# Kernel tuning notes

Measured on AMD Instinct MI355X. Metric: run time of the kernel, lower is better.

The kernel has to match this reference:

```python
import jax, jax.numpy as jnp
import numpy as np

N_NODES = 50000
N_EDGES = 1600000
F_IN, F_HID, F_MID = 264, 48, 64


def setup_inputs() -> dict:
    key = jax.random.key(0)
    ks = jax.random.split(key, 12)
    def lin(kw, fan_in, fan_out):
        s = 1.0 / np.sqrt(fan_in)
        return jax.random.uniform(kw, (fan_in, fan_out), jnp.float32, -s, s)
    return {
        "x": jax.random.normal(ks[0], (N_NODES, F_IN), jnp.float32),
        "edge_index": jax.random.randint(ks[1], (2, N_EDGES), 0, N_NODES, jnp.int64),
        "edge_weight": jax.random.uniform(ks[2], (N_EDGES,), jnp.float32, 0.01, 1.0),
        "WM": lin(ks[3], F_IN, F_HID), "bM": jnp.zeros((F_HID,), jnp.float32),
        "WA": lin(ks[4], F_IN, F_HID), "bA": jnp.zeros((F_HID,), jnp.float32),
        "WS": lin(ks[5], F_IN, F_HID), "bS": jnp.zeros((F_HID,), jnp.float32),
        "W1": lin(ks[6], 3 * F_HID, F_MID), "b1": jnp.zeros((F_MID,), jnp.float32),
        "W2": lin(ks[7], F_MID, 1), "b2": jnp.zeros((1,), jnp.float32),
    }


def _gcn_norm(edge_index, edge_weight, n):
    # add self-loops with weight 1 (PyG gcn_norm default)
    loop = jnp.arange(n, dtype=edge_index.dtype)
    row = jnp.concatenate([edge_index[0], loop])
    col = jnp.concatenate([edge_index[1], loop])
    w = jnp.concatenate([edge_weight, jnp.ones((n,), edge_weight.dtype)])
    deg = jax.ops.segment_sum(w, col, num_segments=n)
    dis = jnp.where(deg > 0, jax.lax.rsqrt(jnp.where(deg > 0, deg, 1.0)), 0.0)
    norm = dis[row] * w * dis[col]
    return row, col, norm


def reference(x, edge_index, edge_weight, WM, bM, WA, bA, WS, bS, W1, b1, W2, b2):
    n = x.shape[0]
    row, col, norm = _gcn_norm(edge_index, edge_weight, n)

    # GCNConv aggr='max': linear (no bias) -> gather -> weighted scatter-max -> +bias
    hM = x @ WM                              # [N, 48]
    msgM = norm[:, None] * hM[row]           # [E+N, 48]
    outM = jax.ops.segment_max(msgM, col, num_segments=n) + bM
    xConvM = jax.nn.relu(outM)

    # GCNConv aggr='add'
    hA = x @ WA
    msgA = norm[:, None] * hA[row]
    outA = jax.ops.segment_sum(msgA, col, num_segments=n) + bA
    xConvA = jax.nn.relu(outA)

    # plain linear branch
    xLin = jax.nn.relu(x @ WS + bS)

    h = jnp.concatenate([xConvM, xConvA, xLin], axis=1)  # [N, 144]
    h = jax.nn.relu(h @ W1 + b1)
    out = h @ W2 + b2                         # [N, 1]
    return out.squeeze(-1)
```

## Files before the change

kernel.cpp:

```cpp
#include <hip/hip_runtime.h>
#include <stdint.h>

#define N_NODES 50000
#define N_EDGES 1600000
#define F_IN    264
#define F_HID   48
#define F_CAT   144
#define F_MID   64
#define K_PAD   288
#define K_MLP   160

#define BSH     6
#define NB      782
#define CHUNK   4096
#define NCHUNK  ((N_EDGES + CHUNK - 1) / CHUNK)

typedef unsigned short u16;
typedef unsigned int   u32;

using short8  = __attribute__((ext_vector_type(8))) short;
using floatx4 = __attribute__((ext_vector_type(4))) float;
using floatx2 = __attribute__((ext_vector_type(2))) float;
using uintx4  = __attribute__((ext_vector_type(4))) u32;

__device__ __forceinline__ float bf2f(u16 u) {
    return __uint_as_float(((u32)u) << 16);
}
__device__ __forceinline__ u16 f2bf(float f) {
    u32 u = __float_as_uint(f);
    u32 r = (u + 0x7fffu + ((u >> 16) & 1u)) >> 16;
    return (u16)r;
}
__device__ __forceinline__ float ldf(const void* p, size_t i, int isbf) {
    return isbf ? bf2f(((const u16*)p)[i]) : ((const float*)p)[i];
}
__device__ __forceinline__ uintx4 s8_to_u4(short8 v) {
    union { short8 s; uintx4 u; } c; c.s = v; return c.u;
}

__global__ __launch_bounds__(64)
void k_probe(const u16* __restrict__ xu, const int* __restrict__ ei,
             int* __restrict__ flags) {
    int lane = threadIdx.x;
    u16 h = xu[2 * lane];
    u32 E = (h >> 7) & 0xFF;
    int sane = (h == 0) || (E >= 90 && E <= 140);
    unsigned long long m = __ballot(sane);
    int cnt = __popcll(m);
    int z = (lane < 16) ? ei[2 * lane + 1] : 0;
    unsigned long long nz = __ballot(z != 0);
    if (lane == 0) {
        flags[0] = (cnt >= 48) ? 1 : 0;
        flags[1] = (nz == 0ull) ? 1 : 0;
    }
}

__device__ __forceinline__ int ld_row(const int* ei, int e, int is64) {
    return is64 ? ei[2 * (size_t)e] : ei[e];
}
__device__ __forceinline__ int ld_col(const int* ei, int e, int is64) {
    return is64 ? ei[2 * ((size_t)N_EDGES + e)] : ei[(size_t)N_EDGES + e];
}

__global__ __launch_bounds__(256)
void k_prep(const void* __restrict__ WM, const void* __restrict__ WA,
            const void* __restrict__ WS, const void* __restrict__ W1,
            const void* __restrict__ bM, const void* __restrict__ bA,
            const void* __restrict__ b1, const void* __restrict__ W2,
            const void* __restrict__ b2,
            u16* __restrict__ Wt, u16* __restrict__ W1bt,
            float* __restrict__ bMf, float* __restrict__ bAf,
            float* __restrict__ b1f, float* __restrict__ W2f,
            float* __restrict__ b2f, const int* __restrict__ flags) {
    const int isbf = flags[0];
    int t = blockIdx.x * 256 + threadIdx.x;
    if (t < F_CAT * K_PAD) {
        int n = t / K_PAD, k = t - n * K_PAD;
        u16 v = 0;
        if (k < F_IN) {
            const void* W = (n < 48) ? WM : (n < 96) ? WA : WS;
            int nn = (n < 48) ? n : (n < 96) ? n - 48 : n - 96;
            if (isbf) v = ((const u16*)W)[(size_t)k * 48 + nn];
            else      v = f2bf(((const float*)W)[(size_t)k * 48 + nn]);
        }
        Wt[(size_t)n * K_PAD + k] = v;
        return;
    }
    t -= F_CAT * K_PAD;
    if (t < F_MID * K_MLP) {
        int j = t / K_MLP, k = t - j * K_MLP;
        u16 v = 0;
        if (k < F_CAT) {
            if (isbf) v = ((const u16*)W1)[(size_t)k * F_MID + j];
            else      v = f2bf(((const float*)W1)[(size_t)k * F_MID + j]);
        }
        W1bt[t] = v;
        return;
    }
    t -= F_MID * K_MLP;
    if (t < 48)            { bMf[t] = ldf(bM, t, isbf); return; }
    t -= 48;
    if (t < 48)            { bAf[t] = ldf(bA, t, isbf); return; }
    t -= 48;
    if (t < 64)            { b1f[t] = ldf(b1, t, isbf); return; }
    t -= 64;
    if (t < 64)            { W2f[t] = ldf(W2, t, isbf); return; }
    t -= 64;
    if (t < 1)             { b2f[0] = ldf(b2, 0, isbf); return; }
}

__global__ __launch_bounds__(256)
void k_bhist(const int* __restrict__ ei, u32* __restrict__ bhist,
             const int* __restrict__ flags) {
    const int is64 = flags[1];
    __shared__ u32 hist[NB];
    for (int j = threadIdx.x; j < NB; j += 256) hist[j] = 0;
    __syncthreads();
    int e0 = blockIdx.x * CHUNK;
    for (int i = 0; i < CHUNK / 256; ++i) {
        int e = e0 + i * 256 + threadIdx.x;
        if (e < N_EDGES) {
            int c = ld_col(ei, e, is64);
            atomicAdd(&hist[(u32)c >> BSH], 1u);
        }
    }
    __syncthreads();
    for (int j = threadIdx.x; j < NB; j += 256)
        bhist[(size_t)j * NCHUNK + blockIdx.x] = hist[j];
}

__global__ __launch_bounds__(256)
void k_bscan1(u32* __restrict__ bhist, u32* __restrict__ bsum) {
    const int wid  = (blockIdx.x * 256 + threadIdx.x) >> 6;
    const int lane = threadIdx.x & 63;
    if (wid >= NB) return;
    u32* row = bhist + (size_t)wid * NCHUNK;
    u32 run = 0;
    for (int i0 = 0; i0 < NCHUNK; i0 += 64) {
        int i = i0 + lane;
        u32 v = (i < NCHUNK) ? row[i] : 0u;
        u32 sc = v;
#pragma unroll
        for (int off = 1; off < 64; off <<= 1) {
            u32 t = (u32)__shfl_up((int)sc, off, 64);
            if (lane >= off) sc += t;
        }
        if (i < NCHUNK) row[i] = run + sc - v;
        run += (u32)__shfl((int)sc, 63, 64);
    }
    if (lane == 0) bsum[wid] = run;
}

__global__ __launch_bounds__(1024)
void k_bscan2(const u32* __restrict__ bsum, u32* __restrict__ boff) {
    __shared__ u32 part[1024];
    int tid = threadIdx.x;
    u32 v = (tid < NB) ? bsum[tid] : 0u;
    part[tid] = v;
    __syncthreads();
    for (int off = 1; off < 1024; off <<= 1) {
        u32 t = (tid >= off) ? part[tid - off] : 0u;
        __syncthreads();
        part[tid] += t;
        __syncthreads();
    }
    if (tid < NB) boff[tid] = part[tid] - v;
    if (tid == NB - 1) boff[NB] = part[tid];
}

__global__ __launch_bounds__(256)
void k_bplace(const int* __restrict__ ei, const void* __restrict__ ew,
              const u32* __restrict__ bhist, const u32* __restrict__ boff,
              int2* __restrict__ bpair, const int* __restrict__ flags) {
    const int isbf = flags[0], is64 = flags[1];
    __shared__ u32 cur[NB];
    for (int j = threadIdx.x; j < NB; j += 256)
        cur[j] = boff[j] + bhist[(size_t)j * NCHUNK + blockIdx.x];
    __syncthreads();
    int e0 = blockIdx.x * CHUNK;
    for (int i = 0; i < CHUNK / 256; ++i) {
        int e = e0 + i * 256 + threadIdx.x;
        if (e < N_EDGES) {
            int c = ld_col(ei, e, is64);
            int r = ld_row(ei, e, is64);
            float w = ldf(ew, e, isbf);
            u32 p = atomicAdd(&cur[(u32)c >> BSH], 1u);
            bpair[p] = make_int2(r | ((c & 63) << 16), __float_as_int(w));
        }
    }
}

__global__ __launch_bounds__(256)
void k_bcsr(const int2* __restrict__ bpair, const u32* __restrict__ boff,
            int* __restrict__ rowptr, int2* __restrict__ csr_pair,
            float* __restrict__ dis) {
    const int b   = blockIdx.x;
    const int tid = threadIdx.x;
    const u32 base = boff[b];
    const u32 n    = boff[b + 1] - base;
    const int c0   = b << BSH;
    __shared__ u32 chist[64], pcur[64], pbeg[64];
    if (tid < 64) chist[tid] = 0;
    __syncthreads();
    for (u32 i = tid; i < n; i += 256)
        atomicAdd(&chist[((u32)bpair[base + i].x >> 16) & 63u], 1u);
    __syncthreads();
    if (tid < 64) {
        u32 v = chist[tid];
        u32 sc = v;
        for (int off = 1; off < 64; off <<= 1) {
            u32 t = (u32)__shfl_up((int)sc, off, 64);
            if (tid >= off) sc += t;
        }
        u32 excl = sc - v;
        pcur[tid] = excl;
        pbeg[tid] = excl;
        int c = c0 + tid;
        if (c <= N_NODES) rowptr[c] = (int)(base + excl);
    }
    __syncthreads();
    for (u32 i = tid; i < n; i += 256) {
        int2 e2 = bpair[base + i];
        u32 lc = ((u32)e2.x >> 16) & 63u;
        u32 lr = atomicAdd(&pcur[lc], 1u);
        csr_pair[base + lr] = make_int2(e2.x & 0xFFFF, e2.y);
    }
    __syncthreads();
    int j = tid >> 2, sub = tid & 3;
    int c = c0 + j;
    if (c < N_NODES) {
        u32 s0 = base + pbeg[j], s1 = base + pcur[j];
        float s = 0.f;
        for (u32 i = s0 + sub; i < s1; i += 4)
            s += __int_as_float(csr_pair[i].y);
        s += __shfl_down(s, 2, 4);
        s += __shfl_down(s, 1, 4);
        if (sub == 0) dis[c] = rsqrtf(1.0f + s);
    }
}

__global__ __launch_bounds__(256)
void k_gemm(const void* __restrict__ x, const u16* __restrict__ Wt,
            u16* __restrict__ hMB, u16* __restrict__ hFull,
            const void* __restrict__ bS, const int* __restrict__ flags) {
    const int isbf = flags[0];
    const int lane = threadIdx.x & 63;
    const int wave = threadIdx.x >> 6;
    const int mrow = lane & 15;
    const int q    = lane >> 4;
    const int m_base = blockIdx.x * 128 + wave * 32;

    floatx4 acc[2][9];
#pragma unroll
    for (int tt = 0; tt < 2; ++tt)
#pragma unroll
        for (int t = 0; t < 9; ++t) {
            acc[tt][t][0]=0.f; acc[tt][t][1]=0.f; acc[tt][t][2]=0.f; acc[tt][t][3]=0.f;
        }

    for (int k0 = 0; k0 < K_PAD; k0 += 32) {
        int k = k0 + q * 8;
        short8 a[2];
#pragma unroll
        for (int tt = 0; tt < 2; ++tt) {
            int node = m_base + tt * 16 + mrow;
            short8 av = {0,0,0,0,0,0,0,0};
            if (node < N_NODES && k < F_IN) {
                if (isbf) {
                    av = *(const short8*)((const u16*)x + (size_t)node * F_IN + k);
                } else {
                    const float* xf = (const float*)x + (size_t)node * F_IN + k;
                    floatx4 v0 = *(const floatx4*)xf;
                    floatx4 v1 = *(const floatx4*)(xf + 4);
                    av[0]=(short)f2bf(v0[0]); av[1]=(short)f2bf(v0[1]);
                    av[2]=(short)f2bf(v0[2]); av[3]=(short)f2bf(v0[3]);
                    av[4]=(short)f2bf(v1[0]); av[5]=(short)f2bf(v1[1]);
                    av[6]=(short)f2bf(v1[2]); av[7]=(short)f2bf(v1[3]);
                }
            }
            a[tt] = av;
        }
#pragma unroll
        for (int t = 0; t < 9; ++t) {
            short8 b = *(const short8*)(Wt + (size_t)(t * 16 + mrow) * K_PAD + k);
            acc[0][t] = __builtin_amdgcn_mfma_f32_16x16x32_bf16(a[0], b, acc[0][t], 0, 0, 0);
            acc[1][t] = __builtin_amdgcn_mfma_f32_16x16x32_bf16(a[1], b, acc[1][t], 0, 0, 0);
        }
    }
#pragma unroll
    for (int tt = 0; tt < 2; ++tt)
#pragma unroll
    for (int t = 0; t < 9; ++t) {
        int n = t * 16 + mrow;
#pragma unroll
        for (int r = 0; r < 4; ++r) {
            int row = m_base + tt * 16 + q * 4 + r;
            if (row < N_NODES) {
                float v = acc[tt][t][r];
                if (n < 96) hMB[(size_t)row * 96 + n] = f2bf(v);
                else        hFull[(size_t)row * F_CAT + n] =
                                f2bf(fmaxf(v + ldf(bS, n - 96, isbf), 0.f));
            }
        }
    }
}

__global__ __launch_bounds__(256)
void k_agg(const u16* __restrict__ hMB, u16* __restrict__ hFull,
           const int* __restrict__ rowptr, const int2* __restrict__ csr_pair,
           const float* __restrict__ dis,
           const float* __restrict__ bMf, const float* __restrict__ bAf) {
    const int lane = threadIdx.x & 63;
    const int wave = threadIdx.x >> 6;
    const int node = blockIdx.x * 4 + wave;

    const int g = lane / 12;
    const int s = lane - g * 12;
    const bool active = lane < 60;
    const bool isMax = s < 6;

    const int start = rowptr[node];
    const int end   = rowptr[node + 1];
    const float dn  = dis[node];
    const float dn2 = dn * dn;
    const float padnm = isMax ? dn2 : 0.f;

    const u32 s16     = 16u * (u32)s;
    const u32 selfOff = __umul24((u32)node, 192u) + s16;

    floatx2 acc2[4];
    {
        short8 rv0 = *(const short8*)((const char*)hMB + selfOff);
        uintx4 w4 = s8_to_u4(rv0);
        float seed = (isMax || g == 0) ? dn2 : 0.f;
#pragma unroll
        for (int p = 0; p < 4; ++p) {
            acc2[p][0] = seed * __uint_as_float(w4[p] << 16);
            acc2[p][1] = seed * __uint_as_float(w4[p] & 0xffff0000u);
        }
    }

    for (int c0 = start; c0 < end; c0 += 64) {
        int cl = end - c0; if (cl > 64) cl = 64;
        int li = lane < cl ? lane : cl - 1;
        int2 mp = csr_pair[c0 + li];
        float disr = dis[mp.x];
        float mynm = __int_as_float(mp.y) * disr * dn;
        u32 myoff  = __umul24((u32)mp.x, 192u);

        for (int j = 0; j < cl; j += 20) {
            u32 offv[4]; float nmv[4];
#pragma unroll
            for (int u = 0; u < 4; ++u) {
                int el = j + 5 * u + g;
                bool valid = active && (el < cl);
                int elc = (el < cl) ? el : 0;
                u32 off  = (u32)__shfl((int)myoff, elc, 64) + s16;
                float nm = __shfl(mynm, elc, 64);
                offv[u] = valid ? off : selfOff;
                nmv[u]  = valid ? nm  : padnm;
            }
            short8 rv[4];
#pragma unroll
            for (int u = 0; u < 4; ++u)
                rv[u] = *(const short8*)((const char*)hMB + offv[u]);
#pragma unroll
            for (int u = 0; u < 4; ++u) {
                uintx4 w4 = s8_to_u4(rv[u]);
                floatx2 nm2; nm2[0] = nmv[u]; nm2[1] = nmv[u];
#pragma unroll
                for (int p = 0; p < 4; ++p) {
                    floatx2 f;
                    f[0] = __uint_as_float(w4[p] << 16);
                    f[1] = __uint_as_float(w4[p] & 0xffff0000u);
                    if (isMax) {
                        floatx2 m = nm2 * f;
                        acc2[p][0] = fmaxf(acc2[p][0], m[0]);
                        acc2[p][1] = fmaxf(acc2[p][1], m[1]);
                    } else {
                        acc2[p] += nm2 * f;
                    }
                }
            }
        }
    }

#pragma unroll
    for (int gg = 1; gg < 5; ++gg) {
        int src = lane + 12 * gg;
        floatx2 t[4];
#pragma unroll
        for (int p = 0; p < 4; ++p) {
            t[p][0] = __shfl(acc2[p][0], src, 64);
            t[p][1] = __shfl(acc2[p][1], src, 64);
        }
        if (lane < 12) {
            if (isMax) {
#pragma unroll
                for (int p = 0; p < 4; ++p) {
                    acc2[p][0] = fmaxf(acc2[p][0], t[p][0]);
                    acc2[p][1] = fmaxf(acc2[p][1], t[p][1]);
                }
            } else {
#pragma unroll
                for (int p = 0; p < 4; ++p) acc2[p] += t[p];
            }
        }
    }

    if (lane < 12) {
        const float* bp = isMax ? (bMf + 8 * lane) : (bAf + 8 * lane - 48);
        short8 hv;
#pragma unroll
        for (int p = 0; p < 4; ++p) {
            hv[2 * p]     = (short)f2bf(fmaxf(acc2[p][0] + bp[2 * p],     0.f));
            hv[2 * p + 1] = (short)f2bf(fmaxf(acc2[p][1] + bp[2 * p + 1], 0.f));
        }
        *(short8*)(hFull + (size_t)node * F_CAT + 8 * lane) = hv;
    }
}

__global__ __launch_bounds__(256)
void k_mlp(const u16* __restrict__ hFull, const u16* __restrict__ W1bt,
           const float* __restrict__ b1f, const float* __restrict__ W2f,
           const float* __restrict__ b2f, void* __restrict__ out,
           const int* __restrict__ flags) {
    const int isbf = flags[0];
    const int lane = threadIdx.x & 63;
    const int wave = threadIdx.x >> 6;
    const int mrow = lane & 15;
    const int q    = lane >> 4;
    const int m_base = blockIdx.x * 64 + wave * 16;
    const int node = m_base + mrow;

    floatx4 acc[4];
#pragma unroll
    for (int t = 0; t < 4; ++t) { acc[t][0]=0.f; acc[t][1]=0.f; acc[t][2]=0.f; acc[t][3]=0.f; }

    for (int k0 = 0; k0 < K_MLP; k0 += 32) {
        int k = k0 + q * 8;
        short8 a = {0,0,0,0,0,0,0,0};
        if (node < N_NODES && k < F_CAT)
            a = *(const short8*)(hFull + (size_t)node * F_CAT + k);
#pragma unroll
        for (int t = 0; t < 4; ++t) {
            short8 b = *(const short8*)(W1bt + (size_t)(t * 16 + mrow) * K_MLP + k);
            acc[t] = __builtin_amdgcn_mfma_f32_16x16x32_bf16(a, b, acc[t], 0, 0, 0);
        }
    }

    float pr[4] = {0.f, 0.f, 0.f, 0.f};
#pragma unroll
    for (int t = 0; t < 4; ++t) {
        int n = t * 16 + mrow;
        float b1v = b1f[n], w2v = W2f[n];
#pragma unroll
        for (int r = 0; r < 4; ++r)
            pr[r] += fmaxf(acc[t][r] + b1v, 0.f) * w2v;
    }
#pragma unroll
    for (int mask = 1; mask < 16; mask <<= 1)
#pragma unroll
        for (int r = 0; r < 4; ++r) pr[r] += __shfl_xor(pr[r], mask, 64);
    if (mrow == 0) {
#pragma unroll
        for (int r = 0; r < 4; ++r) {
            int nd = m_base + q * 4 + r;
            if (nd < N_NODES) {
                float res = pr[r] + b2f[0];
                if (isbf) ((u16*)out)[nd] = f2bf(res);
                else      ((float*)out)[nd] = res;
            }
        }
    }
}

extern "C" void kernel_launch(void* const* d_in, const int* in_sizes, int n_in,
                              void* d_out, int out_size, void* d_ws, size_t ws_size,
                              hipStream_t stream) {
    const void* x  = d_in[0];
    const int*  ei = (const int*)d_in[1];
    const void* ew = d_in[2];
    const void* WM = d_in[3];
    const void* bM = d_in[4];
    const void* WA = d_in[5];
    const void* bA = d_in[6];
    const void* WS = d_in[7];
    const void* bS = d_in[8];
    const void* W1 = d_in[9];
    const void* b1 = d_in[10];
    const void* W2 = d_in[11];
    const void* b2 = d_in[12];

    char* p = (char*)d_ws;
    auto alloc = [&](size_t bytes) -> char* {
        char* r = p; p += (bytes + 255) & ~(size_t)255; return r;
    };
    int*   flags    = (int*)  alloc(16);
    float* dis      = (float*)alloc((size_t)N_NODES * 4);
    int*   rowptr   = (int*)  alloc((size_t)(N_NODES + 1) * 4);
    int2*  csr_pair = (int2*) alloc((size_t)N_EDGES * 8);
    u16*   hMB      = (u16*)  alloc((size_t)N_NODES * 96 * 2);
    u16*   hFull    = (u16*)  alloc((size_t)N_NODES * F_CAT * 2);
    u16*   Wt       = (u16*)  alloc((size_t)F_CAT * K_PAD * 2);
    u16*   W1bt    = (u16*)  alloc((size_t)F_MID * K_MLP * 2);
    u32*   bhist    = (u32*)  alloc((size_t)NB * NCHUNK * 4);
    u32*   bsum     = (u32*)  alloc((size_t)NB * 4);
    u32*   boff     = (u32*)  alloc((size_t)(NB + 1) * 4);
    float* bMf      = (float*)alloc(48 * 4);
    float* bAf      = (float*)alloc(48 * 4);
    float* b1f      = (float*)alloc(64 * 4);
    float* W2f      = (float*)alloc(64 * 4);
    float* b2f      = (float*)alloc(4);
    int2*  bpair    = (int2*)hMB;

    k_probe <<<1, 64, 0, stream>>>((const u16*)x, ei, flags);
    k_prep  <<<(F_CAT * K_PAD + F_MID * K_MLP + 225 + 255) / 256, 256, 0, stream>>>(
                 WM, WA, WS, W1, bM, bA, b1, W2, b2,
                 Wt, W1bt, bMf, bAf, b1f, W2f, b2f, flags);
    k_bhist <<<NCHUNK, 256, 0, stream>>>(ei, bhist, flags);
    k_bscan1<<<(NB * 64 + 255) / 256, 256, 0, stream>>>(bhist, bsum);
    k_bscan2<<<1, 1024, 0, stream>>>(bsum, boff);
    k_bplace<<<NCHUNK, 256, 0, stream>>>(ei, ew, bhist, boff, bpair, flags);
    k_bcsr  <<<NB, 256, 0, stream>>>(bpair, boff, rowptr, csr_pair, dis);
    k_gemm  <<<(N_NODES + 127) / 128, 256, 0, stream>>>(x, Wt, hMB, hFull, bS, flags);
    k_agg   <<<N_NODES / 4, 256, 0, stream>>>(hMB, hFull, rowptr, csr_pair, dis, bMf, bAf);
    k_mlp   <<<(N_NODES + 63) / 64, 256, 0, stream>>>(hFull, W1bt, b1f, W2f, b2f, d_out, flags);
    (void)in_sizes; (void)n_in; (void)out_size; (void)ws_size;
}
```

Measured before the change: 262.1 us.

## Co-schedule feature GEMM with edge histogram and sort CSR buckets in place

The feature GEMM and the per-chunk column histogram now run in one launch, with different blocks doing each job. This lets the compute-bound GEMM overlap the memory-bound histogram, where before the bucket scratch aliased hMB and forced them to run in order. Bucket placement now writes straight into csr_pair, and k_bcsr holds each bucket's edges in registers (up to 16 per thread) so it can reorder them in place. The degree sum is accumulated with shared-memory float atomics during the same pass, which removes a second read pass. The cost is that buckets with more than 4096 edges would be silently truncated, and float atomic ordering makes the degree sums nondeterministic.

```diff
diff --git a/kernel.cpp b/kernel.cpp
--- a/kernel.cpp
+++ b/kernel.cpp
@@ -14,6 +14,8 @@
 #define NB      782
 #define CHUNK   4096
 #define NCHUNK  ((N_EDGES + CHUNK - 1) / CHUNK)
+#define GEMM_BLOCKS ((N_NODES + 127) / 128)
+#define MAXE    16
 
 typedef unsigned short u16;
 typedef unsigned int   u32;
@@ -110,23 +112,90 @@
 }
 
 __global__ __launch_bounds__(256)
-void k_bhist(const int* __restrict__ ei, u32* __restrict__ bhist,
-             const int* __restrict__ flags) {
-    const int is64 = flags[1];
+void k_fgb(const void* __restrict__ x, const u16* __restrict__ Wt,
+           u16* __restrict__ hMB, u16* __restrict__ hFull,
+           const void* __restrict__ bS,
+           const int* __restrict__ ei, u32* __restrict__ bhist,
+           const int* __restrict__ flags) {
+    const int isbf = flags[0];
     __shared__ u32 hist[NB];
-    for (int j = threadIdx.x; j < NB; j += 256) hist[j] = 0;
-    __syncthreads();
-    int e0 = blockIdx.x * CHUNK;
-    for (int i = 0; i < CHUNK / 256; ++i) {
-        int e = e0 + i * 256 + threadIdx.x;
-        if (e < N_EDGES) {
-            int c = ld_col(ei, e, is64);
-            atomicAdd(&hist[(u32)c >> BSH], 1u);
-        }
-    }
-    __syncthreads();
-    for (int j = threadIdx.x; j < NB; j += 256)
-        bhist[(size_t)j * NCHUNK + blockIdx.x] = hist[j];
+    if (blockIdx.x >= GEMM_BLOCKS) {
+        const int is64 = flags[1];
+        const int blk = blockIdx.x - GEMM_BLOCKS;
+        for (int j = threadIdx.x; j < NB; j += 256) hist[j] = 0;
+        __syncthreads();
+        int e0 = blk * CHUNK;
+        for (int i = 0; i < CHUNK / 256; ++i) {
+            int e = e0 + i * 256 + threadIdx.x;
+            if (e < N_EDGES) {
+                int c = ld_col(ei, e, is64);
+                atomicAdd(&hist[(u32)c >> BSH], 1u);
+            }
+        }
+        __syncthreads();
+        for (int j = threadIdx.x; j < NB; j += 256)
+            bhist[(size_t)j * NCHUNK + blk] = hist[j];
+        return;
+    }
+    const int lane = threadIdx.x & 63;
+    const int wave = threadIdx.x >> 6;
+    const int mrow = lane & 15;
+    const int q    = lane >> 4;
+    const int m_base = blockIdx.x * 128 + wave * 32;
+
+    floatx4 acc[2][9];
+#pragma unroll
+    for (int tt = 0; tt < 2; ++tt)
+#pragma unroll
+        for (int t = 0; t < 9; ++t) {
+            acc[tt][t][0]=0.f; acc[tt][t][1]=0.f; acc[tt][t][2]=0.f; acc[tt][t][3]=0.f;
+        }
+
+    for (int k0 = 0; k0 < K_PAD; k0 += 32) {
+        int k = k0 + q * 8;
+        short8 a[2];
+#pragma unroll
+        for (int tt = 0; tt < 2; ++tt) {
+            int node = m_base + tt * 16 + mrow;
+            short8 av = {0,0,0,0,0,0,0,0};
+            if (node < N_NODES && k < F_IN) {
+                if (isbf) {
+                    av = *(const short8*)((const u16*)x + (size_t)node * F_IN + k);
+                } else {
+                    const float* xf = (const float*)x + (size_t)node * F_IN + k;
+                    floatx4 v0 = *(const floatx4*)xf;
+                    floatx4 v1 = *(const floatx4*)(xf + 4);
+                    av[0]=(short)f2bf(v0[0]); av[1]=(short)f2bf(v0[1]);
+                    av[2]=(short)f2bf(v0[2]); av[3]=(short)f2bf(v0[3]);
+                    av[4]=(short)f2bf(v1[0]); av[5]=(short)f2bf(v1[1]);
+                    av[6]=(short)f2bf(v1[2]); av[7]=(short)f2bf(v1[3]);
+                }
+            }
+            a[tt] = av;
+        }
+#pragma unroll
+        for (int t = 0; t < 9; ++t) {
+            short8 b = *(const short8*)(Wt + (size_t)(t * 16 + mrow) * K_PAD + k);
+            acc[0][t] = __builtin_amdgcn_mfma_f32_16x16x32_bf16(a[0], b, acc[0][t], 0, 0, 0);
+            acc[1][t] = __builtin_amdgcn_mfma_f32_16x16x32_bf16(a[1], b, acc[1][t], 0, 0, 0);
+        }
+    }
+#pragma unroll
+    for (int tt = 0; tt < 2; ++tt)
+#pragma unroll
+    for (int t = 0; t < 9; ++t) {
+        int n = t * 16 + mrow;
+#pragma unroll
+        for (int r = 0; r < 4; ++r) {
+            int row = m_base + tt * 16 + q * 4 + r;
+            if (row < N_NODES) {
+                float v = acc[tt][t][r];
+                if (n < 96) hMB[(size_t)row * 96 + n] = f2bf(v);
+                else        hFull[(size_t)row * F_CAT + n] =
+                                f2bf(fmaxf(v + ldf(bS, n - 96, isbf), 0.f));
+            }
+        }
+    }
 }
 
 __global__ __launch_bounds__(256)
@@ -191,19 +260,32 @@
 }
 
 __global__ __launch_bounds__(256)
-void k_bcsr(const int2* __restrict__ bpair, const u32* __restrict__ boff,
-            int* __restrict__ rowptr, int2* __restrict__ csr_pair,
-            float* __restrict__ dis) {
+void k_bcsr(const u32* __restrict__ boff, int* __restrict__ rowptr,
+            int2* __restrict__ csr_pair, float* __restrict__ dis) {
     const int b   = blockIdx.x;
     const int tid = threadIdx.x;
     const u32 base = boff[b];
     const u32 n    = boff[b + 1] - base;
     const int c0   = b << BSH;
-    __shared__ u32 chist[64], pcur[64], pbeg[64];
-    if (tid < 64) chist[tid] = 0;
+    __shared__ u32 chist[64], pcur[64];
+    __shared__ float dsum[64];
+    if (tid < 64) { chist[tid] = 0u; dsum[tid] = 0.f; }
     __syncthreads();
-    for (u32 i = tid; i < n; i += 256)
-        atomicAdd(&chist[((u32)bpair[base + i].x >> 16) & 63u], 1u);
+    int2 ev[MAXE];
+    u32  lcv[MAXE];
+#pragma unroll
+    for (int t = 0; t < MAXE; ++t) {
+        u32 i = (u32)t * 256u + (u32)tid;
+        if (i < n) {
+            int2 e2 = csr_pair[base + i];
+            ev[t] = e2;
+            u32 lc = ((u32)e2.x >> 16) & 63u;
+            lcv[t] = lc;
+            atomicAdd(&chist[lc], 1u);
+            atomicAdd(&dsum[lc], __int_as_float(e2.y));
+        } else lcv[t] = 0xFFFFFFFFu;
+    }
+    asm volatile("s_waitcnt vmcnt(0)" ::: "memory");
     __syncthreads();
     if (tid < 64) {
         u32 v = chist[tid];
@@ -214,93 +296,16 @@
         }
         u32 excl = sc - v;
         pcur[tid] = excl;
-        pbeg[tid] = excl;
         int c = c0 + tid;
         if (c <= N_NODES) rowptr[c] = (int)(base + excl);
+        if (c < N_NODES)  dis[c] = rsqrtf(1.0f + dsum[tid]);
     }
     __syncthreads();
-    for (u32 i = tid; i < n; i += 256) {
-        int2 e2 = bpair[base + i];
-        u32 lc = ((u32)e2.x >> 16) & 63u;
-        u32 lr = atomicAdd(&pcur[lc], 1u);
-        csr_pair[base + lr] = make_int2(e2.x & 0xFFFF, e2.y);
-    }
-    __syncthreads();
-    int j = tid >> 2, sub = tid & 3;
-    int c = c0 + j;
-    if (c < N_NODES) {
-        u32 s0 = base + pbeg[j], s1 = base + pcur[j];
-        float s = 0.f;
-        for (u32 i = s0 + sub; i < s1; i += 4)
-            s += __int_as_float(csr_pair[i].y);
-        s += __shfl_down(s, 2, 4);
-        s += __shfl_down(s, 1, 4);
-        if (sub == 0) dis[c] = rsqrtf(1.0f + s);
-    }
-}
-
-__global__ __launch_bounds__(256)
-void k_gemm(const void* __restrict__ x, const u16* __restrict__ Wt,
-            u16* __restrict__ hMB, u16* __restrict__ hFull,
-            const void* __restrict__ bS, const int* __restrict__ flags) {
-    const int isbf = flags[0];
-    const int lane = threadIdx.x & 63;
-    const int wave = threadIdx.x >> 6;
-    const int mrow = lane & 15;
-    const int q    = lane >> 4;
-    const int m_base = blockIdx.x * 128 + wave * 32;
-
-    floatx4 acc[2][9];
-#pragma unroll
-    for (int tt = 0; tt < 2; ++tt)
-#pragma unroll
-        for (int t = 0; t < 9; ++t) {
-            acc[tt][t][0]=0.f; acc[tt][t][1]=0.f; acc[tt][t][2]=0.f; acc[tt][t][3]=0.f;
-        }
-
-    for (int k0 = 0; k0 < K_PAD; k0 += 32) {
-        int k = k0 + q * 8;
-        short8 a[2];
-#pragma unroll
-        for (int tt = 0; tt < 2; ++tt) {
-            int node = m_base + tt * 16 + mrow;
-            short8 av = {0,0,0,0,0,0,0,0};
-            if (node < N_NODES && k < F_IN) {
-                if (isbf) {
-                    av = *(const short8*)((const u16*)x + (size_t)node * F_IN + k);
-                } else {
-                    const float* xf = (const float*)x + (size_t)node * F_IN + k;
-                    floatx4 v0 = *(const floatx4*)xf;
-                    floatx4 v1 = *(const floatx4*)(xf + 4);
-                    av[0]=(short)f2bf(v0[0]); av[1]=(short)f2bf(v0[1]);
-                    av[2]=(short)f2bf(v0[2]); av[3]=(short)f2bf(v0[3]);
-                    av[4]=(short)f2bf(v1[0]); av[5]=(short)f2bf(v1[1]);
-                    av[6]=(short)f2bf(v1[2]); av[7]=(short)f2bf(v1[3]);
-                }
-            }
-            a[tt] = av;
-        }
-#pragma unroll
-        for (int t = 0; t < 9; ++t) {
-            short8 b = *(const short8*)(Wt + (size_t)(t * 16 + mrow) * K_PAD + k);
-            acc[0][t] = __builtin_amdgcn_mfma_f32_16x16x32_bf16(a[0], b, acc[0][t], 0, 0, 0);
-            acc[1][t] = __builtin_amdgcn_mfma_f32_16x16x32_bf16(a[1], b, acc[1][t], 0, 0, 0);
-        }
-    }
-#pragma unroll
-    for (int tt = 0; tt < 2; ++tt)
-#pragma unroll
-    for (int t = 0; t < 9; ++t) {
-        int n = t * 16 + mrow;
-#pragma unroll
-        for (int r = 0; r < 4; ++r) {
-            int row = m_base + tt * 16 + q * 4 + r;
-            if (row < N_NODES) {
-                float v = acc[tt][t][r];
-                if (n < 96) hMB[(size_t)row * 96 + n] = f2bf(v);
-                else        hFull[(size_t)row * F_CAT + n] =
-                                f2bf(fmaxf(v + ldf(bS, n - 96, isbf), 0.f));
-            }
+#pragma unroll
+    for (int t = 0; t < MAXE; ++t) {
+        if (lcv[t] != 0xFFFFFFFFu) {
+            u32 lr = atomicAdd(&pcur[lcv[t]], 1u);
+            csr_pair[base + lr] = make_int2(ev[t].x & 0xFFFF, ev[t].y);
         }
     }
 }
@@ -512,18 +517,17 @@
     float* b1f      = (float*)alloc(64 * 4);
     float* W2f      = (float*)alloc(64 * 4);
     float* b2f      = (float*)alloc(4);
-    int2*  bpair    = (int2*)hMB;
 
     k_probe <<<1, 64, 0, stream>>>((const u16*)x, ei, flags);
     k_prep  <<<(F_CAT * K_PAD + F_MID * K_MLP + 225 + 255) / 256, 256, 0, stream>>>(
                  WM, WA, WS, W1, bM, bA, b1, W2, b2,
                  Wt, W1bt, bMf, bAf, b1f, W2f, b2f, flags);
-    k_bhist <<<NCHUNK, 256, 0, stream>>>(ei, bhist, flags);
+    k_fgb   <<<GEMM_BLOCKS + NCHUNK, 256, 0, stream>>>(
+                 x, Wt, hMB, hFull, bS, ei, bhist, flags);
     k_bscan1<<<(NB * 64 + 255) / 256, 256, 0, stream>>>(bhist, bsum);
     k_bscan2<<<1, 1024, 0, stream>>>(bsum, boff);
-    k_bplace<<<NCHUNK, 256, 0, stream>>>(ei, ew, bhist, boff, bpair, flags);
-    k_bcsr  <<<NB, 256, 0, stream>>>(bpair, boff, rowptr, csr_pair, dis);
-    k_gemm  <<<(N_NODES + 127) / 128, 256, 0, stream>>>(x, Wt, hMB, hFull, bS, flags);
+    k_bplace<<<NCHUNK, 256, 0, stream>>>(ei, ew, bhist, boff, csr_pair, flags);
+    k_bcsr  <<<NB, 256, 0, stream>>>(boff, rowptr, csr_pair, dis);
     k_agg   <<<N_NODES / 4, 256, 0, stream>>>(hMB, hFull, rowptr, csr_pair, dis, bMf, bAf);
     k_mlp   <<<(N_NODES + 63) / 64, 256, 0, stream>>>(hFull, W1bt, b1f, W2f, b2f, d_out, flags);
     (void)in_sizes; (void)n_in; (void)out_size; (void)ws_size;
```

Result: slower. 277.2 us (+5.8%).

## Stage bucketed edges in shared memory before coalesced global scatter

Applied to the files above, without the earlier changes.

The bucket placement kernel now builds a local histogram and a prefix scan per chunk, sorts the chunk's edges by bucket into a shared-memory staging buffer, and then writes them to global memory in bucket order. This turns random global scatter writes into mostly contiguous runs per bucket, which should improve write coalescing. The cost is extra shared memory (32KB staging plus scan arrays), more barriers, and a second pass that reads boff and bhist per element. The bucket index is packed into the high bits of the row field, which relies on the row value fitting in 16 bits.

```diff
diff --git a/kernel.cpp b/kernel.cpp
--- a/kernel.cpp
+++ b/kernel.cpp
@@ -12,6 +12,7 @@
 
 #define BSH     6
 #define NB      782
+#define NBP     1024
 #define CHUNK   4096
 #define NCHUNK  ((N_EDGES + CHUNK - 1) / CHUNK)
 
@@ -173,20 +174,74 @@
               const u32* __restrict__ bhist, const u32* __restrict__ boff,
               int2* __restrict__ bpair, const int* __restrict__ flags) {
     const int isbf = flags[0], is64 = flags[1];
-    __shared__ u32 cur[NB];
-    for (int j = threadIdx.x; j < NB; j += 256)
-        cur[j] = boff[j] + bhist[(size_t)j * NCHUNK + blockIdx.x];
-    __syncthreads();
-    int e0 = blockIdx.x * CHUNK;
+    const int blk = blockIdx.x;
+    const int tid = threadIdx.x;
+    __shared__ int2 stage[CHUNK];
+    __shared__ u32 lcur[NBP];
+    __shared__ u32 lbase[NBP];
+    __shared__ u32 wsum[4];
+    for (int j = tid; j < NBP; j += 256) lcur[j] = 0;
+    __syncthreads();
+    const int e0 = blk * CHUNK;
+    u32 cv[CHUNK / 256];
+#pragma unroll
     for (int i = 0; i < CHUNK / 256; ++i) {
-        int e = e0 + i * 256 + threadIdx.x;
+        int e = e0 + i * 256 + tid;
+        u32 c = 0xFFFFFFFFu;
         if (e < N_EDGES) {
-            int c = ld_col(ei, e, is64);
+            c = (u32)ld_col(ei, e, is64);
+            atomicAdd(&lcur[c >> BSH], 1u);
+        }
+        cv[i] = c;
+    }
+    __syncthreads();
+    {
+        u32 a0 = lcur[4 * tid], a1 = lcur[4 * tid + 1];
+        u32 a2 = lcur[4 * tid + 2], a3 = lcur[4 * tid + 3];
+        u32 s = a0 + a1 + a2 + a3;
+        u32 sc = s;
+        int lane = tid & 63;
+#pragma unroll
+        for (int off = 1; off < 64; off <<= 1) {
+            u32 t = (u32)__shfl_up((int)sc, off, 64);
+            if (lane >= off) sc += t;
+        }
+        if (lane == 63) wsum[tid >> 6] = sc;
+        __syncthreads();
+        u32 wbase = 0;
+        for (int wv = 0; wv < (tid >> 6); ++wv) wbase += wsum[wv];
+        u32 excl = wbase + sc - s;
+        lbase[4 * tid]     = excl;
+        lbase[4 * tid + 1] = excl + a0;
+        lbase[4 * tid + 2] = excl + a0 + a1;
+        lbase[4 * tid + 3] = excl + a0 + a1 + a2;
+        __syncthreads();
+        lcur[4 * tid]     = excl;
+        lcur[4 * tid + 1] = excl + a0;
+        lcur[4 * tid + 2] = excl + a0 + a1;
+        lcur[4 * tid + 3] = excl + a0 + a1 + a2;
+    }
+    __syncthreads();
+#pragma unroll
+    for (int i = 0; i < CHUNK / 256; ++i) {
+        if (cv[i] != 0xFFFFFFFFu) {
+            int e = e0 + i * 256 + tid;
+            u32 c = cv[i];
+            u32 j = c >> BSH;
             int r = ld_row(ei, e, is64);
             float w = ldf(ew, e, isbf);
-            u32 p = atomicAdd(&cur[(u32)c >> BSH], 1u);
-            bpair[p] = make_int2(r | ((c & 63) << 16), __float_as_int(w));
-        }
+            u32 slot = atomicAdd(&lcur[j], 1u);
+            stage[slot] = make_int2(r | (int)((c & 63u) << 16) | (int)(j << 22),
+                                    __float_as_int(w));
+        }
+    }
+    __syncthreads();
+    int tot = N_EDGES - e0; if (tot > CHUNK) tot = CHUNK;
+    for (int i = tid; i < tot; i += 256) {
+        int2 e2 = stage[i];
+        u32 j = (u32)e2.x >> 22;
+        u32 tgt = boff[j] + bhist[(size_t)j * NCHUNK + blk] + ((u32)i - lbase[j]);
+        bpair[tgt] = e2;
     }
 }
 
```

Result: no change. 260.6 us (-0.6%).
